# Kernel tuning notes

Hardware: AMD Instinct MI355X
Metric: run time of the kernel (lower is better)

The kernel has to match this reference:

```python
import jax, jax.numpy as jnp
import numpy as np

P, K, C = 20000, 16, 100


def setup_inputs() -> dict:
    key = jax.random.key(0)
    k1, k2, k3, k4, k5 = jax.random.split(key, 5)
    pnts = jax.random.normal(k1, (P, 3), dtype=jnp.float32)
    Lnbrs = jax.random.randint(k2, (P, K), 0, P)
    Lwgts = jax.random.uniform(k3, (P, K), dtype=jnp.float32)
    Ldiag = -jnp.sum(Lwgts, axis=-1)  # matches Ldiag = -sum(Lwgts) in __init__
    crhs = jax.random.normal(k4, (C, 3), dtype=jnp.float32)
    # dense pseudo-inverse stand-in; scaled small to keep iterates numerically tame
    iA = jax.random.normal(k5, (P + C, P + C), dtype=jnp.float32) * 1e-3
    return {"pnts": pnts, "Lnbrs": Lnbrs, "Lwgts": Lwgts, "Ldiag": Ldiag,
            "crhs": crhs, "iA": iA, "num_iter": 2}


def _mul_L(x, Lnbrs, Lwgts, Ldiag):
    # weighted neighbor gather-reduce + diagonal term: (P,3)
    return jnp.sum(x[Lnbrs] * Lwgts[..., None], axis=1) + Ldiag[..., None] * x


def _estimate_rhs(old_pnts, new_pnts, Lnbrs, Lwgts, Ldiag):
    # edge vectors weighted by Laplacian weights: (P,K,3)
    O = -(old_pnts[Lnbrs] - old_pnts[:, None, :]) * Lwgts[:, :, None]
    N = -(new_pnts[Lnbrs] - new_pnts[:, None, :]) * Lwgts[:, :, None]
    cov = jnp.einsum('pki,pkj->pij', N, O)           # N^T @ O per vertex: (P,3,3)
    U, s, Vt = jnp.linalg.svd(cov, full_matrices=False)
    sign = jnp.sign(jnp.linalg.det(U @ Vt))
    ones = jnp.ones_like(sign)
    s_new = jnp.stack([ones, ones, sign], axis=-1)   # (P,3)
    R = U @ (s_new[..., None] * Vt)                  # proper rotation fit: (P,3,3)
    Rsum = R[Lnbrs] + R[:, None, :, :]               # (P,K,3,3)
    d_new = jnp.sum(jnp.einsum('pkij,pkj->pki', Rsum, O) * (0.5 * Lwgts[:, :, None]),
                    axis=1)                          # (P,3)
    return _mul_L(d_new, Lnbrs, Lwgts, Ldiag)


def reference(pnts, Lnbrs, Lwgts, Ldiag, crhs, iA, num_iter):
    lrhs = _mul_L(_mul_L(pnts, Lnbrs, Lwgts, Ldiag), Lnbrs, Lwgts, Ldiag)
    rhs = jnp.concatenate([lrhs, crhs], axis=0)      # (P+C,3)
    new_pnts = (iA @ rhs)[:P]
    for _ in range(num_iter):
        new_rhs = _estimate_rhs(pnts, new_pnts, Lnbrs, Lwgts, Ldiag)
        rhs = jnp.concatenate([new_rhs, crhs], axis=0)
        new_pnts = (iA @ rhs)[:P]
    return new_pnts
```

## Files before the change

kernel.cpp:

```cpp
#include <hip/hip_runtime.h>

#define P_N   20000
#define K_N   16
#define C_N   100
#define NCOL  20100
#define NC4   5025
#define NUM_ITER 2
#define ROWS  8

typedef float f4 __attribute__((ext_vector_type(4)));

__global__ __launch_bounds__(256) void mul_L_kernel(const float* __restrict__ x,
    const int* __restrict__ nbrs, const float* __restrict__ wgts,
    const float* __restrict__ diag, float* __restrict__ out) {
  int p = blockIdx.x * blockDim.x + threadIdx.x;
  if (p >= P_N) return;
  float xx = x[3*p], xy = x[3*p+1], xz = x[3*p+2];
  float ax = 0.f, ay = 0.f, az = 0.f;
  #pragma unroll
  for (int k = 0; k < K_N; ++k) {
    int nb = nbrs[p*K_N + k];
    float w = wgts[p*K_N + k];
    ax += x[3*nb]   * w;
    ay += x[3*nb+1] * w;
    az += x[3*nb+2] * w;
  }
  float d = diag[p];
  out[3*p]   = ax + d*xx;
  out[3*p+1] = ay + d*xy;
  out[3*p+2] = az + d*xz;
}

__global__ __launch_bounds__(256) void mulL_pack_kernel(const float* __restrict__ x,
    const int* __restrict__ nbrs, const float* __restrict__ wgts,
    const float* __restrict__ diag, const float* __restrict__ crhs,
    float* __restrict__ rhsT) {
  int j = blockIdx.x * blockDim.x + threadIdx.x;
  if (j >= NCOL) return;
  float v0, v1, v2;
  if (j < P_N) {
    float xx = x[3*j], xy = x[3*j+1], xz = x[3*j+2];
    float ax = 0.f, ay = 0.f, az = 0.f;
    #pragma unroll
    for (int k = 0; k < K_N; ++k) {
      int nb = nbrs[j*K_N + k];
      float w = wgts[j*K_N + k];
      ax += x[3*nb]   * w;
      ay += x[3*nb+1] * w;
      az += x[3*nb+2] * w;
    }
    float d = diag[j];
    v0 = ax + d*xx; v1 = ay + d*xy; v2 = az + d*xz;
  } else {
    int q = j - P_N;
    v0 = crhs[3*q]; v1 = crhs[3*q+1]; v2 = crhs[3*q+2];
  }
  rhsT[j] = v0; rhsT[NCOL + j] = v1; rhsT[2*NCOL + j] = v2;
}

__global__ __launch_bounds__(256) void matvec_kernel(const float* __restrict__ A,
    const float* __restrict__ rhsT, float* __restrict__ out) {
  int row0 = blockIdx.x * ROWS;
  const f4* __restrict__ Ablk = reinterpret_cast<const f4*>(A) + (size_t)row0 * NC4;
  const f4* __restrict__ r0 = reinterpret_cast<const f4*>(rhsT);
  const f4* __restrict__ r1 = reinterpret_cast<const f4*>(rhsT + NCOL);
  const f4* __restrict__ r2 = reinterpret_cast<const f4*>(rhsT + 2*NCOL);
  float acc[ROWS][3];
  #pragma unroll
  for (int r = 0; r < ROWS; ++r) { acc[r][0] = 0.f; acc[r][1] = 0.f; acc[r][2] = 0.f; }
  for (int j = threadIdx.x; j < NC4; j += 256) {
    f4 b0 = r0[j];
    f4 b1 = r1[j];
    f4 b2 = r2[j];
    #pragma unroll
    for (int r = 0; r < ROWS; ++r) {
      f4 a = __builtin_nontemporal_load(Ablk + (size_t)r * NC4 + j);
      acc[r][0] = fmaf(a.x,b0.x, fmaf(a.y,b0.y, fmaf(a.z,b0.z, fmaf(a.w,b0.w, acc[r][0]))));
      acc[r][1] = fmaf(a.x,b1.x, fmaf(a.y,b1.y, fmaf(a.z,b1.z, fmaf(a.w,b1.w, acc[r][1]))));
      acc[r][2] = fmaf(a.x,b2.x, fmaf(a.y,b2.y, fmaf(a.z,b2.z, fmaf(a.w,b2.w, acc[r][2]))));
    }
  }
  #pragma unroll
  for (int off = 32; off > 0; off >>= 1) {
    #pragma unroll
    for (int r = 0; r < ROWS; ++r) {
      acc[r][0] += __shfl_down(acc[r][0], off);
      acc[r][1] += __shfl_down(acc[r][1], off);
      acc[r][2] += __shfl_down(acc[r][2], off);
    }
  }
  __shared__ float red[4][ROWS][3];
  int wid = threadIdx.x >> 6, lane = threadIdx.x & 63;
  if (lane == 0) {
    #pragma unroll
    for (int r = 0; r < ROWS; ++r) {
      red[wid][r][0] = acc[r][0];
      red[wid][r][1] = acc[r][1];
      red[wid][r][2] = acc[r][2];
    }
  }
  __syncthreads();
  if (threadIdx.x < ROWS*3) {
    int r = threadIdx.x / 3, c = threadIdx.x % 3;
    float s = red[0][r][c] + red[1][r][c] + red[2][r][c] + red[3][r][c];
    out[3*(row0+r)+c] = s;
  }
}

template<int PP, int QQ, int RR>
__device__ __forceinline__ void jacobi_rot(float S[3][3], float V[3][3]) {
  float apq = S[PP][QQ];
  if (fabsf(apq) < 1e-30f) return;
  float app = S[PP][PP], aqq = S[QQ][QQ];
  float tau = (aqq - app) / (2.0f * apq);
  float t = (tau >= 0.f ? 1.f : -1.f) / (fabsf(tau) + sqrtf(1.f + tau*tau));
  float c = 1.0f / sqrtf(1.f + t*t);
  float s = t * c;
  float arp = S[PP][RR], arq = S[QQ][RR];
  float npp = c*c*app - 2.f*s*c*apq + s*s*aqq;
  float nqq = s*s*app + 2.f*s*c*apq + c*c*aqq;
  S[PP][PP] = npp; S[QQ][QQ] = nqq;
  S[PP][QQ] = 0.f; S[QQ][PP] = 0.f;
  float narp = c*arp - s*arq;
  float narq = s*arp + c*arq;
  S[PP][RR] = narp; S[RR][PP] = narp;
  S[QQ][RR] = narq; S[RR][QQ] = narq;
  #pragma unroll
  for (int i = 0; i < 3; ++i) {
    float vp = V[i][PP], vq = V[i][QQ];
    V[i][PP] = c*vp - s*vq;
    V[i][QQ] = s*vp + c*vq;
  }
}

__global__ __launch_bounds__(256) void compute_R_kernel(const float* __restrict__ oldp,
    const float* __restrict__ newp, const int* __restrict__ nbrs,
    const float* __restrict__ wgts, float* __restrict__ Rout) {
  int p = blockIdx.x * blockDim.x + threadIdx.x;
  if (p >= P_N) return;
  float ox = oldp[3*p], oy = oldp[3*p+1], oz = oldp[3*p+2];
  float nx = newp[3*p], ny = newp[3*p+1], nz = newp[3*p+2];
  float c00=0,c01=0,c02=0,c10=0,c11=0,c12=0,c20=0,c21=0,c22=0;
  #pragma unroll
  for (int k = 0; k < K_N; ++k) {
    int nb = nbrs[p*K_N + k];
    float w = wgts[p*K_N + k];
    float Ox = (ox - oldp[3*nb])   * w;
    float Oy = (oy - oldp[3*nb+1]) * w;
    float Oz = (oz - oldp[3*nb+2]) * w;
    float Nx = (nx - newp[3*nb])   * w;
    float Ny = (ny - newp[3*nb+1]) * w;
    float Nz = (nz - newp[3*nb+2]) * w;
    c00 += Nx*Ox; c01 += Nx*Oy; c02 += Nx*Oz;
    c10 += Ny*Ox; c11 += Ny*Oy; c12 += Ny*Oz;
    c20 += Nz*Ox; c21 += Nz*Oy; c22 += Nz*Oz;
  }
  float S[3][3];
  S[0][0] = c00*c00 + c10*c10 + c20*c20;
  S[1][1] = c01*c01 + c11*c11 + c21*c21;
  S[2][2] = c02*c02 + c12*c12 + c22*c22;
  S[0][1] = c00*c01 + c10*c11 + c20*c21; S[1][0] = S[0][1];
  S[0][2] = c00*c02 + c10*c12 + c20*c22; S[2][0] = S[0][2];
  S[1][2] = c01*c02 + c11*c12 + c21*c22; S[2][1] = S[1][2];
  float V[3][3] = {{1.f,0.f,0.f},{0.f,1.f,0.f},{0.f,0.f,1.f}};
  #pragma unroll
  for (int sweep = 0; sweep < 8; ++sweep) {
    jacobi_rot<0,1,2>(S, V);
    jacobi_rot<0,2,1>(S, V);
    jacobi_rot<1,2,0>(S, V);
  }
  float e0 = S[0][0], e1 = S[1][1], e2 = S[2][2];
  float v0x=V[0][0], v0y=V[1][0], v0z=V[2][0];
  float v1x=V[0][1], v1y=V[1][1], v1z=V[2][1];
  float v2x=V[0][2], v2y=V[1][2], v2z=V[2][2];
  float te, tx, ty, tz;
  if (e1 > e0) { te=e0;e0=e1;e1=te; tx=v0x;ty=v0y;tz=v0z; v0x=v1x;v0y=v1y;v0z=v1z; v1x=tx;v1y=ty;v1z=tz; }
  if (e2 > e0) { te=e0;e0=e2;e2=te; tx=v0x;ty=v0y;tz=v0z; v0x=v2x;v0y=v2y;v0z=v2z; v2x=tx;v2y=ty;v2z=tz; }
  if (e2 > e1) { te=e1;e1=e2;e2=te; tx=v1x;ty=v1y;tz=v1z; v1x=v2x;v1y=v2y;v1z=v2z; v2x=tx;v2y=ty;v2z=tz; }
  float u0x = c00*v0x + c01*v0y + c02*v0z;
  float u0y = c10*v0x + c11*v0y + c12*v0z;
  float u0z = c20*v0x + c21*v0y + c22*v0z;
  float n0 = sqrtf(u0x*u0x + u0y*u0y + u0z*u0z);
  float R00,R01,R02,R10,R11,R12,R20,R21,R22;
  if (n0 < 1e-25f) {
    R00=1.f;R01=0.f;R02=0.f;R10=0.f;R11=1.f;R12=0.f;R20=0.f;R21=0.f;R22=1.f;
  } else {
    float in0 = 1.f/n0; u0x*=in0; u0y*=in0; u0z*=in0;
    float u1x = c00*v1x + c01*v1y + c02*v1z;
    float u1y = c10*v1x + c11*v1y + c12*v1z;
    float u1z = c20*v1x + c21*v1y + c22*v1z;
    float d01 = u1x*u0x + u1y*u0y + u1z*u0z;
    u1x -= d01*u0x; u1y -= d01*u0y; u1z -= d01*u0z;
    float n1 = sqrtf(u1x*u1x + u1y*u1y + u1z*u1z);
    if (n1 > 1e-6f * n0) {
      float in1 = 1.f/n1; u1x*=in1; u1y*=in1; u1z*=in1;
    } else {
      if (fabsf(u0x) < 0.7f) {
        float nn = 1.f/sqrtf(u0z*u0z + u0y*u0y + 1e-30f);
        u1x = 0.f; u1y = u0z*nn; u1z = -u0y*nn;
      } else {
        float nn = 1.f/sqrtf(u0z*u0z + u0x*u0x + 1e-30f);
        u1x = -u0z*nn; u1y = 0.f; u1z = u0x*nn;
      }
    }
    float u2x = u0y*u1z - u0z*u1y;
    float u2y = u0z*u1x - u0x*u1z;
    float u2z = u0x*u1y - u0y*u1x;
    float detV = v0x*(v1y*v2z - v1z*v2y) - v0y*(v1x*v2z - v1z*v2x) + v0z*(v1x*v2y - v1y*v2x);
    float sg = (detV >= 0.f) ? 1.f : -1.f;
    R00 = u0x*v0x + u1x*v1x + sg*u2x*v2x;
    R01 = u0x*v0y + u1x*v1y + sg*u2x*v2y;
    R02 = u0x*v0z + u1x*v1z + sg*u2x*v2z;
    R10 = u0y*v0x + u1y*v1x + sg*u2y*v2x;
    R11 = u0y*v0y + u1y*v1y + sg*u2y*v2y;
    R12 = u0y*v0z + u1y*v1z + sg*u2y*v2z;
    R20 = u0z*v0x + u1z*v1x + sg*u2z*v2x;
    R21 = u0z*v0y + u1z*v1y + sg*u2z*v2y;
    R22 = u0z*v0z + u1z*v1z + sg*u2z*v2z;
  }
  float* Rp = Rout + (size_t)p * 9;
  Rp[0]=R00; Rp[1]=R01; Rp[2]=R02;
  Rp[3]=R10; Rp[4]=R11; Rp[5]=R12;
  Rp[6]=R20; Rp[7]=R21; Rp[8]=R22;
}

__global__ __launch_bounds__(256) void dnew_kernel(const float* __restrict__ oldp,
    const int* __restrict__ nbrs, const float* __restrict__ wgts,
    const float* __restrict__ Rbuf, float* __restrict__ dnew) {
  int p = blockIdx.x * blockDim.x + threadIdx.x;
  if (p >= P_N) return;
  float ox = oldp[3*p], oy = oldp[3*p+1], oz = oldp[3*p+2];
  const float* Rp = Rbuf + (size_t)p * 9;
  float p00=Rp[0],p01=Rp[1],p02=Rp[2],p10=Rp[3],p11=Rp[4],p12=Rp[5],p20=Rp[6],p21=Rp[7],p22=Rp[8];
  float ax = 0.f, ay = 0.f, az = 0.f;
  #pragma unroll
  for (int k = 0; k < K_N; ++k) {
    int nb = nbrs[p*K_N + k];
    float w = wgts[p*K_N + k];
    float Ox = (ox - oldp[3*nb])   * w;
    float Oy = (oy - oldp[3*nb+1]) * w;
    float Oz = (oz - oldp[3*nb+2]) * w;
    const float* Rn = Rbuf + (size_t)nb * 9;
    float r00=Rn[0]+p00, r01=Rn[1]+p01, r02=Rn[2]+p02;
    float r10=Rn[3]+p10, r11=Rn[4]+p11, r12=Rn[5]+p12;
    float r20=Rn[6]+p20, r21=Rn[7]+p21, r22=Rn[8]+p22;
    float hw = 0.5f * w;
    ax += hw * (r00*Ox + r01*Oy + r02*Oz);
    ay += hw * (r10*Ox + r11*Oy + r12*Oz);
    az += hw * (r20*Ox + r21*Oy + r22*Oz);
  }
  dnew[3*p]   = ax;
  dnew[3*p+1] = ay;
  dnew[3*p+2] = az;
}

extern "C" void kernel_launch(void* const* d_in, const int* in_sizes, int n_in,
                              void* d_out, int out_size, void* d_ws, size_t ws_size,
                              hipStream_t stream) {
  const float* pnts = (const float*)d_in[0];
  const int*   nbrs = (const int*)d_in[1];
  const float* wgts = (const float*)d_in[2];
  const float* diag = (const float*)d_in[3];
  const float* crhs = (const float*)d_in[4];
  const float* iA   = (const float*)d_in[5];
  float* out = (float*)d_out;

  float* ws   = (float*)d_ws;
  float* rhsT = ws;
  float* t1   = ws + 60304;
  float* Rbuf = t1 + 60000;
  dim3 b(256);
  int gp = (P_N  + 255) / 256;
  int gj = (NCOL + 255) / 256;
  int gm = P_N / ROWS;

  mul_L_kernel<<<gp, b, 0, stream>>>(pnts, nbrs, wgts, diag, t1);
  mulL_pack_kernel<<<gj, b, 0, stream>>>(t1, nbrs, wgts, diag, crhs, rhsT);
  matvec_kernel<<<gm, b, 0, stream>>>(iA, rhsT, out);

  for (int it = 0; it < NUM_ITER; ++it) {
    compute_R_kernel<<<gp, b, 0, stream>>>(pnts, out, nbrs, wgts, Rbuf);
    dnew_kernel<<<gp, b, 0, stream>>>(pnts, nbrs, wgts, Rbuf, t1);
    mulL_pack_kernel<<<gj, b, 0, stream>>>(t1, nbrs, wgts, diag, crhs, rhsT);
    matvec_kernel<<<gm, b, 0, stream>>>(iA, rhsT, out);
  }
}
```

Before: 841.7 us.

## Fuse small gather stages into persistent kernels with software grid barriers

The separate mul_L, compute_R, dnew and pack kernels are merged into two chain kernels of 256 blocks that use an atomic-counter grid barrier between dependent stages, cutting the number of launches. The matvec loop is also manually unrolled by two to keep more loads in flight. This depends on all 256 blocks being co-resident for the spin barrier and adds a memset of the counters. The dominant cost remains streaming the large dense matrix three times, so any gain is limited to launch and gap overhead.

Measured after the change: 928.8 us. +10.3%, slower.

```diff
diff --git a/kernel.cpp b/kernel.cpp
--- a/kernel.cpp
+++ b/kernel.cpp
@@ -7,14 +7,24 @@
 #define NC4   5025
 #define NUM_ITER 2
 #define ROWS  8
+#define GB    256
 
 typedef float f4 __attribute__((ext_vector_type(4)));
 
-__global__ __launch_bounds__(256) void mul_L_kernel(const float* __restrict__ x,
+__device__ __forceinline__ void grid_barrier(int* cnt) {
+  __syncthreads();
+  if (threadIdx.x == 0) {
+    __threadfence();
+    atomicAdd(cnt, 1);
+    while (__hip_atomic_load(cnt, __ATOMIC_RELAXED, __HIP_MEMORY_SCOPE_AGENT) < (int)gridDim.x) {}
+    __threadfence();
+  }
+  __syncthreads();
+}
+
+__device__ __forceinline__ void L_apply(int p, const float* __restrict__ x,
     const int* __restrict__ nbrs, const float* __restrict__ wgts,
-    const float* __restrict__ diag, float* __restrict__ out) {
-  int p = blockIdx.x * blockDim.x + threadIdx.x;
-  if (p >= P_N) return;
+    const float* __restrict__ diag, float& v0, float& v1, float& v2) {
   float xx = x[3*p], xy = x[3*p+1], xz = x[3*p+2];
   float ax = 0.f, ay = 0.f, az = 0.f;
   #pragma unroll
@@ -26,85 +36,7 @@
     az += x[3*nb+2] * w;
   }
   float d = diag[p];
-  out[3*p]   = ax + d*xx;
-  out[3*p+1] = ay + d*xy;
-  out[3*p+2] = az + d*xz;
-}
-
-__global__ __launch_bounds__(256) void mulL_pack_kernel(const float* __restrict__ x,
-    const int* __restrict__ nbrs, const float* __restrict__ wgts,
-    const float* __restrict__ diag, const float* __restrict__ crhs,
-    float* __restrict__ rhsT) {
-  int j = blockIdx.x * blockDim.x + threadIdx.x;
-  if (j >= NCOL) return;
-  float v0, v1, v2;
-  if (j < P_N) {
-    float xx = x[3*j], xy = x[3*j+1], xz = x[3*j+2];
-    float ax = 0.f, ay = 0.f, az = 0.f;
-    #pragma unroll
-    for (int k = 0; k < K_N; ++k) {
-      int nb = nbrs[j*K_N + k];
-      float w = wgts[j*K_N + k];
-      ax += x[3*nb]   * w;
-      ay += x[3*nb+1] * w;
-      az += x[3*nb+2] * w;
-    }
-    float d = diag[j];
-    v0 = ax + d*xx; v1 = ay + d*xy; v2 = az + d*xz;
-  } else {
-    int q = j - P_N;
-    v0 = crhs[3*q]; v1 = crhs[3*q+1]; v2 = crhs[3*q+2];
-  }
-  rhsT[j] = v0; rhsT[NCOL + j] = v1; rhsT[2*NCOL + j] = v2;
-}
-
-__global__ __launch_bounds__(256) void matvec_kernel(const float* __restrict__ A,
-    const float* __restrict__ rhsT, float* __restrict__ out) {
-  int row0 = blockIdx.x * ROWS;
-  const f4* __restrict__ Ablk = reinterpret_cast<const f4*>(A) + (size_t)row0 * NC4;
-  const f4* __restrict__ r0 = reinterpret_cast<const f4*>(rhsT);
-  const f4* __restrict__ r1 = reinterpret_cast<const f4*>(rhsT + NCOL);
-  const f4* __restrict__ r2 = reinterpret_cast<const f4*>(rhsT + 2*NCOL);
-  float acc[ROWS][3];
-  #pragma unroll
-  for (int r = 0; r < ROWS; ++r) { acc[r][0] = 0.f; acc[r][1] = 0.f; acc[r][2] = 0.f; }
-  for (int j = threadIdx.x; j < NC4; j += 256) {
-    f4 b0 = r0[j];
-    f4 b1 = r1[j];
-    f4 b2 = r2[j];
-    #pragma unroll
-    for (int r = 0; r < ROWS; ++r) {
-      f4 a = __builtin_nontemporal_load(Ablk + (size_t)r * NC4 + j);
-      acc[r][0] = fmaf(a.x,b0.x, fmaf(a.y,b0.y, fmaf(a.z,b0.z, fmaf(a.w,b0.w, acc[r][0]))));
-      acc[r][1] = fmaf(a.x,b1.x, fmaf(a.y,b1.y, fmaf(a.z,b1.z, fmaf(a.w,b1.w, acc[r][1]))));
-      acc[r][2] = fmaf(a.x,b2.x, fmaf(a.y,b2.y, fmaf(a.z,b2.z, fmaf(a.w,b2.w, acc[r][2]))));
-    }
-  }
-  #pragma unroll
-  for (int off = 32; off > 0; off >>= 1) {
-    #pragma unroll
-    for (int r = 0; r < ROWS; ++r) {
-      acc[r][0] += __shfl_down(acc[r][0], off);
-      acc[r][1] += __shfl_down(acc[r][1], off);
-      acc[r][2] += __shfl_down(acc[r][2], off);
-    }
-  }
-  __shared__ float red[4][ROWS][3];
-  int wid = threadIdx.x >> 6, lane = threadIdx.x & 63;
-  if (lane == 0) {
-    #pragma unroll
-    for (int r = 0; r < ROWS; ++r) {
-      red[wid][r][0] = acc[r][0];
-      red[wid][r][1] = acc[r][1];
-      red[wid][r][2] = acc[r][2];
-    }
-  }
-  __syncthreads();
-  if (threadIdx.x < ROWS*3) {
-    int r = threadIdx.x / 3, c = threadIdx.x % 3;
-    float s = red[0][r][c] + red[1][r][c] + red[2][r][c] + red[3][r][c];
-    out[3*(row0+r)+c] = s;
-  }
+  v0 = ax + d*xx; v1 = ay + d*xy; v2 = az + d*xz;
 }
 
 template<int PP, int QQ, int RR>
@@ -133,11 +65,9 @@
   }
 }
 
-__global__ __launch_bounds__(256) void compute_R_kernel(const float* __restrict__ oldp,
+__device__ __forceinline__ void kabsch_R(int p, const float* __restrict__ oldp,
     const float* __restrict__ newp, const int* __restrict__ nbrs,
     const float* __restrict__ wgts, float* __restrict__ Rout) {
-  int p = blockIdx.x * blockDim.x + threadIdx.x;
-  if (p >= P_N) return;
   float ox = oldp[3*p], oy = oldp[3*p+1], oz = oldp[3*p+2];
   float nx = newp[3*p], ny = newp[3*p+1], nz = newp[3*p+2];
   float c00=0,c01=0,c02=0,c10=0,c11=0,c12=0,c20=0,c21=0,c22=0;
@@ -224,34 +154,126 @@
   Rp[6]=R20; Rp[7]=R21; Rp[8]=R22;
 }
 
-__global__ __launch_bounds__(256) void dnew_kernel(const float* __restrict__ oldp,
+__global__ __launch_bounds__(256) void init_chain_kernel(const float* __restrict__ pnts,
     const int* __restrict__ nbrs, const float* __restrict__ wgts,
-    const float* __restrict__ Rbuf, float* __restrict__ dnew) {
-  int p = blockIdx.x * blockDim.x + threadIdx.x;
-  if (p >= P_N) return;
-  float ox = oldp[3*p], oy = oldp[3*p+1], oz = oldp[3*p+2];
-  const float* Rp = Rbuf + (size_t)p * 9;
-  float p00=Rp[0],p01=Rp[1],p02=Rp[2],p10=Rp[3],p11=Rp[4],p12=Rp[5],p20=Rp[6],p21=Rp[7],p22=Rp[8];
-  float ax = 0.f, ay = 0.f, az = 0.f;
-  #pragma unroll
-  for (int k = 0; k < K_N; ++k) {
-    int nb = nbrs[p*K_N + k];
-    float w = wgts[p*K_N + k];
-    float Ox = (ox - oldp[3*nb])   * w;
-    float Oy = (oy - oldp[3*nb+1]) * w;
-    float Oz = (oz - oldp[3*nb+2]) * w;
-    const float* Rn = Rbuf + (size_t)nb * 9;
-    float r00=Rn[0]+p00, r01=Rn[1]+p01, r02=Rn[2]+p02;
-    float r10=Rn[3]+p10, r11=Rn[4]+p11, r12=Rn[5]+p12;
-    float r20=Rn[6]+p20, r21=Rn[7]+p21, r22=Rn[8]+p22;
-    float hw = 0.5f * w;
-    ax += hw * (r00*Ox + r01*Oy + r02*Oz);
-    ay += hw * (r10*Ox + r11*Oy + r12*Oz);
-    az += hw * (r20*Ox + r21*Oy + r22*Oz);
-  }
-  dnew[3*p]   = ax;
-  dnew[3*p+1] = ay;
-  dnew[3*p+2] = az;
+    const float* __restrict__ diag, const float* __restrict__ crhs,
+    float* __restrict__ t1, float* __restrict__ rhsT, int* __restrict__ cnt) {
+  int t = blockIdx.x * 256 + threadIdx.x;
+  if (t < P_N) {
+    float v0, v1, v2;
+    L_apply(t, pnts, nbrs, wgts, diag, v0, v1, v2);
+    t1[3*t] = v0; t1[3*t+1] = v1; t1[3*t+2] = v2;
+  }
+  grid_barrier(cnt);
+  if (t < NCOL) {
+    float v0, v1, v2;
+    if (t < P_N) L_apply(t, t1, nbrs, wgts, diag, v0, v1, v2);
+    else { int q = t - P_N; v0 = crhs[3*q]; v1 = crhs[3*q+1]; v2 = crhs[3*q+2]; }
+    rhsT[t] = v0; rhsT[NCOL + t] = v1; rhsT[2*NCOL + t] = v2;
+  }
+}
+
+__global__ __launch_bounds__(256) void iter_chain_kernel(const float* __restrict__ pnts,
+    const float* __restrict__ newp, const int* __restrict__ nbrs,
+    const float* __restrict__ wgts, const float* __restrict__ diag,
+    const float* __restrict__ crhs, float* __restrict__ Rbuf,
+    float* __restrict__ t1, float* __restrict__ rhsT, int* __restrict__ cnt) {
+  int t = blockIdx.x * 256 + threadIdx.x;
+  if (t < P_N) kabsch_R(t, pnts, newp, nbrs, wgts, Rbuf);
+  grid_barrier(cnt);
+  if (t < P_N) {
+    int p = t;
+    float ox = pnts[3*p], oy = pnts[3*p+1], oz = pnts[3*p+2];
+    const float* Rp = Rbuf + (size_t)p * 9;
+    float p00=Rp[0],p01=Rp[1],p02=Rp[2],p10=Rp[3],p11=Rp[4],p12=Rp[5],p20=Rp[6],p21=Rp[7],p22=Rp[8];
+    float ax = 0.f, ay = 0.f, az = 0.f;
+    #pragma unroll
+    for (int k = 0; k < K_N; ++k) {
+      int nb = nbrs[p*K_N + k];
+      float w = wgts[p*K_N + k];
+      float Ox = (ox - pnts[3*nb])   * w;
+      float Oy = (oy - pnts[3*nb+1]) * w;
+      float Oz = (oz - pnts[3*nb+2]) * w;
+      const float* Rn = Rbuf + (size_t)nb * 9;
+      float r00=Rn[0]+p00, r01=Rn[1]+p01, r02=Rn[2]+p02;
+      float r10=Rn[3]+p10, r11=Rn[4]+p11, r12=Rn[5]+p12;
+      float r20=Rn[6]+p20, r21=Rn[7]+p21, r22=Rn[8]+p22;
+      float hw = 0.5f * w;
+      ax += hw * (r00*Ox + r01*Oy + r02*Oz);
+      ay += hw * (r10*Ox + r11*Oy + r12*Oz);
+      az += hw * (r20*Ox + r21*Oy + r22*Oz);
+    }
+    t1[3*p]   = ax;
+    t1[3*p+1] = ay;
+    t1[3*p+2] = az;
+  }
+  grid_barrier(cnt + 1);
+  if (t < NCOL) {
+    float v0, v1, v2;
+    if (t < P_N) L_apply(t, t1, nbrs, wgts, diag, v0, v1, v2);
+    else { int q = t - P_N; v0 = crhs[3*q]; v1 = crhs[3*q+1]; v2 = crhs[3*q+2]; }
+    rhsT[t] = v0; rhsT[NCOL + t] = v1; rhsT[2*NCOL + t] = v2;
+  }
+}
+
+__global__ __launch_bounds__(256) void matvec_kernel(const float* __restrict__ A,
+    const float* __restrict__ rhsT, float* __restrict__ out) {
+  int row0 = blockIdx.x * ROWS;
+  const f4* __restrict__ Ablk = reinterpret_cast<const f4*>(A) + (size_t)row0 * NC4;
+  const f4* __restrict__ r0 = reinterpret_cast<const f4*>(rhsT);
+  const f4* __restrict__ r1 = reinterpret_cast<const f4*>(rhsT + NCOL);
+  const f4* __restrict__ r2 = reinterpret_cast<const f4*>(rhsT + 2*NCOL);
+  float acc[ROWS][3];
+  #pragma unroll
+  for (int r = 0; r < ROWS; ++r) { acc[r][0] = 0.f; acc[r][1] = 0.f; acc[r][2] = 0.f; }
+
+#define MV_BODY(J)                                                              \
+  {                                                                             \
+    f4 b0 = r0[(J)];                                                            \
+    f4 b1 = r1[(J)];                                                            \
+    f4 b2 = r2[(J)];                                                            \
+    _Pragma("unroll")                                                           \
+    for (int r = 0; r < ROWS; ++r) {                                            \
+      f4 a = __builtin_nontemporal_load(Ablk + (size_t)r * NC4 + (J));          \
+      acc[r][0] = fmaf(a.x,b0.x, fmaf(a.y,b0.y, fmaf(a.z,b0.z, fmaf(a.w,b0.w, acc[r][0])))); \
+      acc[r][1] = fmaf(a.x,b1.x, fmaf(a.y,b1.y, fmaf(a.z,b1.z, fmaf(a.w,b1.w, acc[r][1])))); \
+      acc[r][2] = fmaf(a.x,b2.x, fmaf(a.y,b2.y, fmaf(a.z,b2.z, fmaf(a.w,b2.w, acc[r][2])))); \
+    }                                                                           \
+  }
+
+  int j = threadIdx.x;
+  for (; j + 256 < NC4; j += 512) {
+    MV_BODY(j);
+    MV_BODY(j + 256);
+  }
+  if (j < NC4) MV_BODY(j);
+#undef MV_BODY
+
+  #pragma unroll
+  for (int off = 32; off > 0; off >>= 1) {
+    #pragma unroll
+    for (int r = 0; r < ROWS; ++r) {
+      acc[r][0] += __shfl_down(acc[r][0], off);
+      acc[r][1] += __shfl_down(acc[r][1], off);
+      acc[r][2] += __shfl_down(acc[r][2], off);
+    }
+  }
+  __shared__ float red[4][ROWS][3];
+  int wid = threadIdx.x >> 6, lane = threadIdx.x & 63;
+  if (lane == 0) {
+    #pragma unroll
+    for (int r = 0; r < ROWS; ++r) {
+      red[wid][r][0] = acc[r][0];
+      red[wid][r][1] = acc[r][1];
+      red[wid][r][2] = acc[r][2];
+    }
+  }
+  __syncthreads();
+  if (threadIdx.x < ROWS*3) {
+    int r = threadIdx.x / 3, c = threadIdx.x % 3;
+    float s = red[0][r][c] + red[1][r][c] + red[2][r][c] + red[3][r][c];
+    out[3*(row0+r)+c] = s;
+  }
 }
 
 extern "C" void kernel_launch(void* const* d_in, const int* in_sizes, int n_in,
@@ -269,19 +291,19 @@
   float* rhsT = ws;
   float* t1   = ws + 60304;
   float* Rbuf = t1 + 60000;
+  int*   cnts = (int*)(Rbuf + 180000);
+
+  hipMemsetAsync(cnts, 0, 8 * sizeof(int), stream);
+
   dim3 b(256);
-  int gp = (P_N  + 255) / 256;
-  int gj = (NCOL + 255) / 256;
   int gm = P_N / ROWS;
 
-  mul_L_kernel<<<gp, b, 0, stream>>>(pnts, nbrs, wgts, diag, t1);
-  mulL_pack_kernel<<<gj, b, 0, stream>>>(t1, nbrs, wgts, diag, crhs, rhsT);
+  init_chain_kernel<<<GB, b, 0, stream>>>(pnts, nbrs, wgts, diag, crhs, t1, rhsT, cnts);
   matvec_kernel<<<gm, b, 0, stream>>>(iA, rhsT, out);
 
-  for (int it = 0; it < NUM_ITER; ++it) {
-    compute_R_kernel<<<gp, b, 0, stream>>>(pnts, out, nbrs, wgts, Rbuf);
-    dnew_kernel<<<gp, b, 0, stream>>>(pnts, nbrs, wgts, Rbuf, t1);
-    mulL_pack_kernel<<<gj, b, 0, stream>>>(t1, nbrs, wgts, diag, crhs, rhsT);
-    matvec_kernel<<<gm, b, 0, stream>>>(iA, rhsT, out);
-  }
-}
+  iter_chain_kernel<<<GB, b, 0, stream>>>(pnts, out, nbrs, wgts, diag, crhs, Rbuf, t1, rhsT, cnts + 1);
+  matvec_kernel<<<gm, b, 0, stream>>>(iA, rhsT, out);
+
+  iter_chain_kernel<<<GB, b, 0, stream>>>(pnts, out, nbrs, wgts, diag, crhs, Rbuf, t1, rhsT, cnts + 3);
+  matvec_kernel<<<gm, b, 0, stream>>>(iA, rhsT, out);
+}
```
